# Performance work log

Measured on AMD Instinct MI355X. Metric: run time of the kernel, lower is better.

Reference implementation:

```python
import jax, jax.numpy as jnp
import numpy as np

D = 256            # number of graph nodes (example.size(3))
K1 = D // 2        # topkpool1 k
K2 = D // 4        # topkpool2 k
B = 8


def _lrelu(x):
    return jnp.where(x > 0, x, 0.33 * x)


def _e2e(h, wa, ba, wb, bb):
    # h: [B,C,d,d]; wa,wb: [P,C,d] (squeezed (1,d)/(d,1) conv kernels)
    # cnn1: contract over columns j -> [B,P,d]; cnn2: contract over rows i -> [B,P,d]
    a = jnp.einsum('bcij,pcj->bpi', h, wa) + ba[None, :, None]
    b = jnp.einsum('bcij,pci->bpj', h, wb) + bb[None, :, None]
    # cat([a]*d, 3) + cat([b]*d, 2)  ==  broadcast-add
    return a[:, :, :, None] + b[:, :, None, :]


def _gcn(h, g, W, b):
    # h: [B,N,F_in], g: [B,N,N]; faithful to norm_g: g[i,j] / deg[j] (column-normalized
    # because torch broadcasts the [N] degree vector over the LAST dim)
    gb = (g > 0).astype(h.dtype)
    deg = gb.sum(axis=2)                      # [B,N] row sums
    gn = gb / deg[:, None, :]                 # divide column j by deg[j]
    return jnp.einsum('bij,bjf->bif', gn, h) @ W.T + b


def _pool(h, g, s, k):
    # h: [B,N,F], g: [B,N,N], s: [B,N,1] -> top-k nodes by score (descending)
    vals, idx = jax.lax.top_k(s[:, :, 0], k)              # [B,k]
    hn = jnp.take_along_axis(h, idx[:, :, None], axis=1)  # [B,k,F]
    gn = jnp.take_along_axis(g, idx[:, :, None], axis=1)
    gn = jnp.take_along_axis(gn, idx[:, None, :], axis=2) # [B,k,k]
    return hn, gn, vals[:, :, None]


def _readout(h):
    # h: [B,N,F] (node axis = 1); torch ReadOut on [B,F,N,1] max/mean over dim=2
    return jnp.concatenate([h.max(axis=1), h.mean(axis=1)], axis=1)  # [B,2F]


def _forward(x, w1a, b1a, w1b, b1b, w2a, b2a, w2b, b2b, e2n_w, e2n_b,
             a11_w, a11_b, a12_w, a12_b, g1_w, g1_b,
             a21_w, a21_b, a22_w, a22_b,
             d1_w, d1_b, d2_w, d2_b, d3_w, d3_b):
    h = _lrelu(_e2e(x, w1a, b1a, w1b, b1b))         # [B,128,d,d]
    h = _lrelu(_e2e(h, w2a, b2a, w2b, b2b))         # [B,256,d,d]
    # E2N conv (1,d): [B,8,d,1] -> node features [B,d,8]
    nodes = _lrelu(jnp.einsum('bcij,pcj->bpi', h, e2n_w) + e2n_b[None, :, None])
    nodes = jnp.transpose(nodes, (0, 2, 1))          # [B,d,8]
    g0 = x[:, 0]                                     # [B,d,d]

    w = _lrelu(_gcn(nodes, g0, a11_w, a11_b))        # [B,d,1]
    w = jax.nn.sigmoid(_gcn(w, g0, a12_w, a12_b))
    h1, g1, s1 = _pool(nodes, g0, w, K1)             # [B,K1,8], [B,K1,K1], [B,K1,1]
    out = h1 * s1 + h1
    sum1 = _readout(out)                             # [B,16]

    h2 = _gcn(out, g1, g1_w, g1_b)                   # [B,K1,8] (no activation, as in torch)
    w = _lrelu(_gcn(h2, g1, a21_w, a21_b))
    w = jax.nn.sigmoid(_gcn(w, g1, a22_w, a22_b))
    h3, g2, s2 = _pool(h2, g1, w, K2)                # [B,K2,8]
    out2 = h3 * s2 + h3
    sum2 = _readout(out2)                            # [B,16]

    z = sum1 + sum2                                  # [B,16]
    z = _lrelu(z @ d1_w.T + d1_b)                    # dropout = identity (eval mode)
    z = _lrelu(z @ d2_w.T + d2_b)
    return z @ d3_w.T + d3_b                         # [B,1]


def setup_inputs() -> dict:
    key = jax.random.key(0)
    ks = jax.random.split(key, 16)
    f32 = jnp.float32

    def rn(k, shape, scale):
        return jax.random.normal(k, shape, dtype=f32) * scale

    return {
        'x': jax.random.normal(ks[0], (B, 1, D, D), dtype=f32),
        'w1a': rn(ks[1], (128, 1, D), 0.08),  'b1a': jnp.zeros((128,), f32),
        'w1b': rn(ks[2], (128, 1, D), 0.08),  'b1b': jnp.zeros((128,), f32),
        'w2a': rn(ks[3], (256, 128, D), 0.008), 'b2a': jnp.zeros((256,), f32),
        'w2b': rn(ks[4], (256, 128, D), 0.008), 'b2b': jnp.zeros((256,), f32),
        'e2n_w': rn(ks[5], (8, 256, D), 0.005), 'e2n_b': jnp.zeros((8,), f32),
        'a11_w': rn(ks[6], (1, 8), 0.3),  'a11_b': jnp.zeros((1,), f32),
        'a12_w': rn(ks[7], (1, 1), 0.3),  'a12_b': jnp.zeros((1,), f32),
        'g1_w': rn(ks[8], (8, 8), 0.3),   'g1_b': jnp.zeros((8,), f32),
        'a21_w': rn(ks[9], (1, 8), 0.3),  'a21_b': jnp.zeros((1,), f32),
        'a22_w': rn(ks[10], (1, 1), 0.3), 'a22_b': jnp.zeros((1,), f32),
        'd1_w': rn(ks[11], (128, 16), 0.2), 'd1_b': jnp.zeros((128,), f32),
        'd2_w': rn(ks[12], (64, 128), 0.08), 'd2_b': jnp.zeros((64,), f32),
        'd3_w': rn(ks[13], (1, 64), 0.1),  'd3_b': jnp.zeros((1,), f32),
    }


def reference(x, w1a, b1a, w1b, b1b, w2a, b2a, w2b, b2b, e2n_w, e2n_b,
              a11_w, a11_b, a12_w, a12_b, g1_w, g1_b,
              a21_w, a21_b, a22_w, a22_b,
              d1_w, d1_b, d2_w, d2_b, d3_w, d3_b):
    return _forward(x, w1a, b1a, w1b, b1b, w2a, b2a, w2b, b2b, e2n_w, e2n_b,
                    a11_w, a11_b, a12_w, a12_b, g1_w, g1_b,
                    a21_w, a21_b, a22_w, a22_b,
                    d1_w, d1_b, d2_w, d2_b, d3_w, d3_b)
```

## Files before the change

### kernel.cpp

```cpp
#include <hip/hip_runtime.h>
#include <hip/hip_bf16.h>

typedef short s16x8 __attribute__((ext_vector_type(8)));
typedef float f32x4 __attribute__((ext_vector_type(4)));
typedef float f32x2 __attribute__((ext_vector_type(2)));

#define TID threadIdx.x
#define N_IN 27

__device__ __forceinline__ float bf2f(unsigned short u) {
    unsigned v = ((unsigned)u) << 16;
    return __builtin_bit_cast(float, v);
}
__device__ __forceinline__ unsigned short f2bf(float f) {
    unsigned u = __builtin_bit_cast(unsigned, f);
    u += 0x7fffu + ((u >> 16) & 1u);
    return (unsigned short)(u >> 16);
}
__device__ __forceinline__ float lrelu_f(float x) { return fmaxf(x, 0.33f * x); }

__device__ __forceinline__ unsigned lrelu_pack(float pv, f32x2 q) {
    f32x2 s = q + pv;
    f32x2 m = s * 0.33f;
    f32x2 r = __builtin_elementwise_max(s, m);
    unsigned u;
    asm("v_cvt_pk_bf16_f32 %0, %1, %2" : "=v"(u) : "v"(r.x), "v"(r.y));
    return u;
}

union FragU { s16x8 v; uint4 q; unsigned w[4]; };

__global__ __launch_bounds__(256) void k_detect(const unsigned* __restrict__ w, int* __restrict__ flag) {
    __shared__ int cnt;
    if (TID == 0) cnt = 0;
    __syncthreads();
    int c = 0;
    for (int k = TID; k < 1024; k += 256) {
        unsigned e = (w[k] >> 23) & 0xFFu;
        c += (e >= 160u) ? 1 : 0;
    }
    atomicAdd(&cnt, c);
    __syncthreads();
    if (TID == 0) *flag = (cnt > 512) ? 1 : 0;
}

struct ConvArgs {
    const void* src[N_IN];
    unsigned short* dst[N_IN];
    int n[N_IN];
};

__global__ __launch_bounds__(256) void k_convert(ConvArgs A, const int* __restrict__ flag) {
    const int t = blockIdx.y;
    const int n = A.n[t];
    const int fl = *flag;
    if (fl && n >= 1000000) return;
    unsigned short* d = A.dst[t];
    const int npair = n >> 1;
    const int stride = gridDim.x * 256;
    if (fl) {
        const unsigned* s = (const unsigned*)A.src[t];
        for (int i = blockIdx.x * 256 + TID; i < npair; i += stride) ((unsigned*)d)[i] = s[i];
        if ((n & 1) && blockIdx.x == 0 && TID == 0) d[n - 1] = ((const unsigned short*)A.src[t])[n - 1];
    } else {
        const float* s = (const float*)A.src[t];
        for (int i = blockIdx.x * 256 + TID; i < npair; i += stride) {
            unsigned u;
            float a = s[2 * i], b = s[2 * i + 1];
            asm("v_cvt_pk_bf16_f32 %0, %1, %2" : "=v"(u) : "v"(a), "v"(b));
            ((unsigned*)d)[i] = u;
        }
        if ((n & 1) && blockIdx.x == 0 && TID == 0) d[n - 1] = f2bf(s[n - 1]);
    }
}

__global__ __launch_bounds__(128) void k_l1(
    const unsigned short* __restrict__ x,
    const unsigned short* __restrict__ w1a, const unsigned short* __restrict__ b1a,
    const unsigned short* __restrict__ w1b, const unsigned short* __restrict__ b1b,
    float* __restrict__ A1, float* __restrict__ B1)
{
    const int r = blockIdx.x, b = blockIdx.y, v = blockIdx.z;
    const int tid = TID;
    __shared__ float xr[256];
    const unsigned short* xb = x + b * 65536;
    if (v == 0) {
        xr[tid]       = bf2f(xb[r * 256 + tid]);
        xr[tid + 128] = bf2f(xb[r * 256 + tid + 128]);
    } else {
        xr[tid]       = bf2f(xb[tid * 256 + r]);
        xr[tid + 128] = bf2f(xb[(tid + 128) * 256 + r]);
    }
    __syncthreads();
    const unsigned short* w    = v ? w1b : w1a;
    const unsigned short* bias = v ? b1b : b1a;
    float* OUT = v ? B1 : A1;
    float acc = bf2f(bias[tid]);
    const unsigned short* wr = w + tid * 256;
    #pragma unroll 4
    for (int q = 0; q < 256; q += 8) {
        uint4 pk = *(const uint4*)(wr + q);
        unsigned ww0 = pk.x, ww1 = pk.y, ww2 = pk.z, ww3 = pk.w;
        acc += xr[q + 0] * bf2f((unsigned short)ww0) + xr[q + 1] * bf2f((unsigned short)(ww0 >> 16));
        acc += xr[q + 2] * bf2f((unsigned short)ww1) + xr[q + 3] * bf2f((unsigned short)(ww1 >> 16));
        acc += xr[q + 4] * bf2f((unsigned short)ww2) + xr[q + 5] * bf2f((unsigned short)(ww2 >> 16));
        acc += xr[q + 6] * bf2f((unsigned short)ww3) + xr[q + 7] * bf2f((unsigned short)(ww3 >> 16));
    }
    OUT[b * 32768 + tid * 256 + r] = acc;
}

__global__ __launch_bounds__(512) void k_e2e(
    const float* __restrict__ A1, const float* __restrict__ B1,
    const unsigned short* __restrict__ w2a_m, const unsigned short* __restrict__ w2b_m,
    const unsigned short* __restrict__ w2a_r, const unsigned short* __restrict__ w2b_r,
    const int* __restrict__ flag,
    float* __restrict__ part)
{
    const int rt = blockIdx.x;
    const int s  = blockIdx.y;
    const int bw = blockIdx.z;
    const int b = bw >> 1, which = bw & 1;
    const int fl = *flag;
    const float* P = (which ? B1 : A1) + b * 32768;
    const float* Q = (which ? A1 : B1) + b * 32768;
    const unsigned short* W = which ? (fl ? w2b_r : w2b_m) : (fl ? w2a_r : w2a_m);
    const int c0 = s * 16, r0 = rt * 128;

    __shared__ float Qs[16][256];
    __shared__ float Ps[16][128];

    const int tid = TID;
    {
        const float4* Qg = (const float4*)(Q + c0 * 256);
        float4* Qd = (float4*)&Qs[0][0];
        Qd[tid]       = Qg[tid];
        Qd[tid + 512] = Qg[tid + 512];
        int row = tid >> 5, col = tid & 31;
        *(float4*)&Ps[row][col * 4] = *(const float4*)&P[(c0 + row) * 256 + r0 + col * 4];
    }
    __syncthreads();

    const int wave = tid >> 6, lane = tid & 63, quad = lane >> 4, l16 = lane & 15;
    const int wi = wave & 3, wj = wave >> 2;
    const int pbase = wi * 64;
    const int rbase = wj * 64;

    f32x4 acc[4][4] = {};

    const unsigned short* Wrow[4];
    #pragma unroll
    for (int pf = 0; pf < 4; ++pf)
        Wrow[pf] = W + (size_t)(pbase + pf * 16 + l16) * 32768 + c0 * 256;

    for (int c = 0; c < 16; ++c) {
        float pv[4];
        #pragma unroll
        for (int nf = 0; nf < 4; ++nf) pv[nf] = Ps[c][rbase + nf * 16 + l16];
        #pragma unroll
        for (int q0 = 0; q0 < 8; ++q0) {
            const f32x2* qp = (const f32x2*)&Qs[c][q0 * 32 + quad * 8];
            FragU af[4];
            #pragma unroll
            for (int pf = 0; pf < 4; ++pf)
                af[pf].q = *(const uint4*)(Wrow[pf] + c * 256 + q0 * 32 + quad * 8);
            #pragma unroll
            for (int nf = 0; nf < 4; ++nf) {
                FragU hb;
                hb.w[0] = lrelu_pack(pv[nf], qp[0]);
                hb.w[1] = lrelu_pack(pv[nf], qp[1]);
                hb.w[2] = lrelu_pack(pv[nf], qp[2]);
                hb.w[3] = lrelu_pack(pv[nf], qp[3]);
                #pragma unroll
                for (int pf = 0; pf < 4; ++pf)
                    acc[pf][nf] = __builtin_amdgcn_mfma_f32_16x16x32_bf16(af[pf].v, hb.v, acc[pf][nf], 0, 0, 0);
            }
        }
    }
    float* pb = part + (size_t)(s * 16 + bw) * 65536;
    #pragma unroll
    for (int pf = 0; pf < 4; ++pf)
        #pragma unroll
        for (int nf = 0; nf < 4; ++nf)
            #pragma unroll
            for (int t = 0; t < 4; ++t) {
                int p = pbase + pf * 16 + quad * 4 + t;
                int r = r0 + rbase + nf * 16 + l16;
                pb[p * 256 + r] = acc[pf][nf][t];
            }
}

__global__ __launch_bounds__(256) void k_red(
    const float* __restrict__ part,
    const unsigned short* __restrict__ b2a, const unsigned short* __restrict__ b2b,
    float* __restrict__ A2, float* __restrict__ B2)
{
    const int bw = blockIdx.y; const int b = bw >> 1, which = bw & 1;
    const int idx = blockIdx.x * 256 + TID;
    const float4* pp = (const float4*)part;
    float4 acc = make_float4(0.f, 0.f, 0.f, 0.f);
    #pragma unroll
    for (int s = 0; s < 8; ++s) {
        float4 v = pp[(size_t)(s * 16 + bw) * 16384 + idx];
        acc.x += v.x; acc.y += v.y; acc.z += v.z; acc.w += v.w;
    }
    const int p = idx >> 6;
    const float bias = bf2f((which ? b2b : b2a)[p]);
    acc.x += bias; acc.y += bias; acc.z += bias; acc.w += bias;
    float* OUT = (which ? B2 : A2) + b * 65536;
    ((float4*)OUT)[idx] = acc;
}

__global__ __launch_bounds__(256) void k_e2n(
    const float* __restrict__ A2, const float* __restrict__ B2,
    const unsigned short* __restrict__ e2nw,
    float* __restrict__ nodes_raw)
{
    const int it = blockIdx.x, b = blockIdx.y, sn = blockIdx.z;
    const int tid = TID, wave = tid >> 6, lane = tid & 63, quad = lane >> 4, l16 = lane & 15;
    const int i0 = it * 16;
    const int c0 = sn * 32 + wave * 8;
    const float* Ab = A2 + b * 65536;
    const float* Bb = B2 + b * 65536;
    f32x4 acc = {};
    for (int cc = 0; cc < 8; ++cc) {
        const int c = c0 + cc;
        const float pv = Ab[c * 256 + i0 + l16];
        const float* Brow = Bb + c * 256;
        const unsigned short* Wrow = e2nw + (size_t)l16 * 65536 + c * 256;
        #pragma unroll
        for (int q0 = 0; q0 < 8; ++q0) {
            const f32x2* qp = (const f32x2*)&Brow[q0 * 32 + quad * 8];
            FragU a;
            if (l16 < 8) a.q = *(const uint4*)(Wrow + q0 * 32 + quad * 8);
            else         a.q = make_uint4(0u, 0u, 0u, 0u);
            FragU hb;
            hb.w[0] = lrelu_pack(pv, qp[0]);
            hb.w[1] = lrelu_pack(pv, qp[1]);
            hb.w[2] = lrelu_pack(pv, qp[2]);
            hb.w[3] = lrelu_pack(pv, qp[3]);
            acc = __builtin_amdgcn_mfma_f32_16x16x32_bf16(a.v, hb.v, acc, 0, 0, 0);
        }
    }
    __shared__ float red[4][16][16];
    #pragma unroll
    for (int t = 0; t < 4; ++t) red[wave][quad * 4 + t][l16] = acc[t];
    __syncthreads();
    const int row = tid >> 4, col = tid & 15;
    if (row < 8) {
        float ssum = red[0][row][col] + red[1][row][col] + red[2][row][col] + red[3][row][col];
        atomicAdd(&nodes_raw[b * 2048 + (i0 + col) * 8 + row], ssum);
    }
}

__global__ __launch_bounds__(256) void k_adj(
    const unsigned short* __restrict__ xm,
    unsigned long long* __restrict__ adjw, float* __restrict__ rdegw)
{
    const int b = blockIdx.y;
    const int tid = TID, wave = tid >> 6, lane = tid & 63;
    const int rbase = blockIdx.x * 32 + wave * 8;
    for (int rr = 0; rr < 8; ++rr) {
        const int row = rbase + rr;
        int d = 0;
        unsigned long long w[4];
        #pragma unroll
        for (int k = 0; k < 4; ++k) {
            float v = bf2f(xm[b * 65536 + row * 256 + k * 64 + lane]);
            w[k] = __ballot(v > 0.0f);
            d += __popcll(w[k]);
        }
        if (lane == 0) {
            #pragma unroll
            for (int k = 0; k < 4; ++k) adjw[(b * 256 + row) * 4 + k] = w[k];
            rdegw[b * 256 + row] = d ? 1.0f / (float)d : 0.0f;
        }
    }
}

__global__ __launch_bounds__(256) void k_tail(
    const unsigned long long* __restrict__ adjw, const float* __restrict__ rdegw,
    const float* __restrict__ nodes_raw, const unsigned short* __restrict__ e2n_b,
    const unsigned short* __restrict__ a11_w, const unsigned short* __restrict__ a11_b,
    const unsigned short* __restrict__ a12_w, const unsigned short* __restrict__ a12_b,
    const unsigned short* __restrict__ g1_w,  const unsigned short* __restrict__ g1_b,
    const unsigned short* __restrict__ a21_w, const unsigned short* __restrict__ a21_b,
    const unsigned short* __restrict__ a22_w, const unsigned short* __restrict__ a22_b,
    const unsigned short* __restrict__ d1_w,  const unsigned short* __restrict__ d1_b,
    const unsigned short* __restrict__ d2_w,  const unsigned short* __restrict__ d2_b,
    const unsigned short* __restrict__ d3_w,  const unsigned short* __restrict__ d3_b,
    const int* __restrict__ flag,
    void* __restrict__ outv)
{
    const int b = blockIdx.x;
    const int tid = TID;

    __shared__ unsigned long long adj[256][4];
    __shared__ float nod[256][8];
    __shared__ float rdeg[256];
    __shared__ float md[256];
    __shared__ float w1s[256];
    __shared__ float w2s[256];
    __shared__ int   selflag[256];
    __shared__ int   selidx[128];
    __shared__ float s1v[128];
    __shared__ float out1[128][8];
    __shared__ float aggL[128][8];
    __shared__ float h2L[128][8];
    __shared__ unsigned long long adj1[128][2];
    __shared__ float rdeg1[128];
    __shared__ float tA[128];
    __shared__ float w1t[128];
    __shared__ float w2t[128];
    __shared__ int   sel2flag[128];
    __shared__ int   sel2idx[64];
    __shared__ float s2v[64];
    __shared__ float out2[64][8];
    __shared__ float r1[16], r2[16], zz[16];
    __shared__ float z1[128];
    __shared__ float z2[64];

    if (tid < 128) { selidx[tid] = 0; s1v[tid] = 0.0f; }
    if (tid < 64)  { sel2idx[tid] = 0; s2v[tid] = 0.0f; }

    {
        #pragma unroll
        for (int k = 0; k < 4; ++k) adj[tid][k] = adjw[(b * 256 + tid) * 4 + k];
        rdeg[tid] = rdegw[b * 256 + tid];
        for (int f = 0; f < 8; ++f)
            nod[tid][f] = lrelu_f(nodes_raw[b * 2048 + tid * 8 + f] + bf2f(e2n_b[f]));
    }
    __syncthreads();
    {
        float s = 0.0f;
        for (int f = 0; f < 8; ++f) s += nod[tid][f] * bf2f(a11_w[f]);
        md[tid] = s * rdeg[tid];
    }
    __syncthreads();
    {
        float s = 0.0f;
        for (int k = 0; k < 4; ++k) {
            unsigned long long m = adj[tid][k];
            while (m) { int j = __builtin_ctzll(m); m &= m - 1; s += md[k * 64 + j]; }
        }
        w1s[tid] = lrelu_f(s + bf2f(a11_b[0]));
    }
    __syncthreads();
    md[tid] = w1s[tid] * bf2f(a12_w[0]) * rdeg[tid];
    __syncthreads();
    {
        float s = 0.0f;
        for (int k = 0; k < 4; ++k) {
            unsigned long long m = adj[tid][k];
            while (m) { int j = __builtin_ctzll(m); m &= m - 1; s += md[k * 64 + j]; }
        }
        w2s[tid] = 1.0f / (1.0f + expf(-(s + bf2f(a12_b[0]))));
    }
    __syncthreads();
    {
        const float my = w2s[tid];
        int cnt = 0;
        for (int j = 0; j < 256; ++j) {
            float o = w2s[j];
            cnt += (o > my) || (o == my && j < tid);
        }
        selflag[tid] = (cnt < 128) ? 1 : 0;
    }
    __syncthreads();
    if (selflag[tid]) {
        int pos = 0;
        for (int j = 0; j < tid; ++j) pos += selflag[j];
        if (pos < 128) { selidx[pos] = tid; s1v[pos] = w2s[tid]; }
    }
    __syncthreads();
    for (int k = tid; k < 1024; k += 256) {
        int t = k >> 3, f = k & 7;
        out1[t][f] = nod[selidx[t]][f] * (1.0f + s1v[t]);
    }
    __syncthreads();
    if (tid < 16) {
        int f = tid & 7;
        if (tid < 8) {
            float mx = -INFINITY;
            for (int t = 0; t < 128; ++t) mx = fmaxf(mx, out1[t][f]);
            r1[tid] = mx;
        } else {
            float s = 0.0f;
            for (int t = 0; t < 128; ++t) s += out1[t][f];
            r1[tid] = s * (1.0f / 128.0f);
        }
    }
    if (tid < 128) {
        unsigned long long wds[2] = {0ull, 0ull};
        const int gi = selidx[tid];
        for (int u = 0; u < 128; ++u) {
            const int gj = selidx[u];
            unsigned long long bit = (adj[gi][gj >> 6] >> (gj & 63)) & 1ull;
            wds[u >> 6] |= bit << (u & 63);
        }
        adj1[tid][0] = wds[0]; adj1[tid][1] = wds[1];
        int d = __popcll(wds[0]) + __popcll(wds[1]);
        rdeg1[tid] = d ? 1.0f / (float)d : 0.0f;
    }
    __syncthreads();
    {
        const int t = tid >> 1, f0 = (tid & 1) * 4;
        float a0 = 0, a1 = 0, a2 = 0, a3 = 0;
        for (int k = 0; k < 2; ++k) {
            unsigned long long m = adj1[t][k];
            while (m) {
                int u = __builtin_ctzll(m); m &= m - 1;
                int uu = k * 64 + u;
                float rr = rdeg1[uu];
                a0 += out1[uu][f0 + 0] * rr;
                a1 += out1[uu][f0 + 1] * rr;
                a2 += out1[uu][f0 + 2] * rr;
                a3 += out1[uu][f0 + 3] * rr;
            }
        }
        aggL[t][f0 + 0] = a0; aggL[t][f0 + 1] = a1; aggL[t][f0 + 2] = a2; aggL[t][f0 + 3] = a3;
    }
    __syncthreads();
    for (int k = tid; k < 1024; k += 256) {
        int t = k >> 3, fo = k & 7;
        float s = bf2f(g1_b[fo]);
        for (int f = 0; f < 8; ++f) s += aggL[t][f] * bf2f(g1_w[fo * 8 + f]);
        h2L[t][fo] = s;
    }
    __syncthreads();
    if (tid < 128) {
        float s = 0.0f;
        for (int f = 0; f < 8; ++f) s += h2L[tid][f] * bf2f(a21_w[f]);
        tA[tid] = s * rdeg1[tid];
    }
    __syncthreads();
    if (tid < 128) {
        float s = 0.0f;
        for (int k = 0; k < 2; ++k) {
            unsigned long long m = adj1[tid][k];
            while (m) { int u = __builtin_ctzll(m); m &= m - 1; s += tA[k * 64 + u]; }
        }
        w1t[tid] = lrelu_f(s + bf2f(a21_b[0]));
    }
    __syncthreads();
    if (tid < 128) tA[tid] = w1t[tid] * bf2f(a22_w[0]) * rdeg1[tid];
    __syncthreads();
    if (tid < 128) {
        float s = 0.0f;
        for (int k = 0; k < 2; ++k) {
            unsigned long long m = adj1[tid][k];
            while (m) { int u = __builtin_ctzll(m); m &= m - 1; s += tA[k * 64 + u]; }
        }
        w2t[tid] = 1.0f / (1.0f + expf(-(s + bf2f(a22_b[0]))));
    }
    __syncthreads();
    if (tid < 128) {
        const float my = w2t[tid];
        int cnt = 0;
        for (int u = 0; u < 128; ++u) {
            float o = w2t[u];
            cnt += (o > my) || (o == my && u < tid);
        }
        sel2flag[tid] = (cnt < 64) ? 1 : 0;
    }
    __syncthreads();
    if (tid < 128 && sel2flag[tid]) {
        int pos = 0;
        for (int u = 0; u < tid; ++u) pos += sel2flag[u];
        if (pos < 64) { sel2idx[pos] = tid; s2v[pos] = w2t[tid]; }
    }
    __syncthreads();
    for (int k = tid; k < 512; k += 256) {
        int u = k >> 3, f = k & 7;
        out2[u][f] = h2L[sel2idx[u]][f] * (1.0f + s2v[u]);
    }
    __syncthreads();
    if (tid < 16) {
        int f = tid & 7;
        if (tid < 8) {
            float mx = -INFINITY;
            for (int t = 0; t < 64; ++t) mx = fmaxf(mx, out2[t][f]);
            r2[tid] = mx;
        } else {
            float s = 0.0f;
            for (int t = 0; t < 64; ++t) s += out2[t][f];
            r2[tid] = s * (1.0f / 64.0f);
        }
    }
    __syncthreads();
    if (tid < 16) zz[tid] = r1[tid] + r2[tid];
    __syncthreads();
    if (tid < 128) {
        float s = bf2f(d1_b[tid]);
        for (int k = 0; k < 16; ++k) s += zz[k] * bf2f(d1_w[tid * 16 + k]);
        z1[tid] = lrelu_f(s);
    }
    __syncthreads();
    if (tid < 64) {
        float s = bf2f(d2_b[tid]);
        for (int k = 0; k < 128; ++k) s += z1[k] * bf2f(d2_w[tid * 128 + k]);
        z2[tid] = lrelu_f(s);
    }
    __syncthreads();
    if (tid == 0) {
        float s = bf2f(d3_b[0]);
        for (int k = 0; k < 64; ++k) s += z2[k] * bf2f(d3_w[k]);
        if (*flag) ((unsigned short*)outv)[b] = f2bf(s);
        else       ((float*)outv)[b] = s;
    }
}

extern "C" void kernel_launch(void* const* d_in, const int* in_sizes, int n_in,
                              void* d_out, int out_size, void* d_ws, size_t ws_size,
                              hipStream_t stream) {
    float* ws        = (float*)d_ws;
    float* A1        = ws;
    float* B1        = ws + 262144;
    float* A2        = ws + 524288;
    float* B2        = ws + 1048576;
    float* nodes_raw = ws + 1572864;
    float* rdegw     = ws + 1589248;
    int*   flag      = (int*)(ws + 1597440);
    unsigned long long* adjw = (unsigned long long*)(ws + 1597444);
    float* part      = ws + 1613832;
    unsigned short* mbase = (unsigned short*)(ws + 10002440);

    unsigned short* mir[N_IN];
    ConvArgs CA;
    {
        size_t off = 0;
        for (int i = 0; i < N_IN; ++i) {
            off = (off + 7) & ~(size_t)7;
            mir[i] = mbase + off;
            off += (size_t)in_sizes[i];
            CA.src[i] = d_in[i];
            CA.dst[i] = mir[i];
            CA.n[i]   = in_sizes[i];
        }
    }

    k_detect<<<dim3(1), 256, 0, stream>>>((const unsigned*)d_in[5], flag);
    k_convert<<<dim3(256, N_IN), 256, 0, stream>>>(CA, flag);
    hipMemsetAsync(nodes_raw, 0, 16384 * sizeof(float), stream);
    k_l1<<<dim3(256, 8, 2), 128, 0, stream>>>(mir[0], mir[1], mir[2], mir[3], mir[4], A1, B1);
    k_adj<<<dim3(8, 8), 256, 0, stream>>>(mir[0], adjw, rdegw);
    k_e2e<<<dim3(2, 8, 16), 512, 0, stream>>>(A1, B1,
        mir[5], mir[7],
        (const unsigned short*)d_in[5], (const unsigned short*)d_in[7],
        flag, part);
    k_red<<<dim3(64, 16), 256, 0, stream>>>(part, mir[6], mir[8], A2, B2);
    k_e2n<<<dim3(16, 8, 8), 256, 0, stream>>>(A2, B2, mir[9], nodes_raw);
    k_tail<<<dim3(8), 256, 0, stream>>>(adjw, rdegw, nodes_raw, mir[10],
        mir[11], mir[12], mir[13], mir[14], mir[15], mir[16], mir[17], mir[18],
        mir[19], mir[20], mir[21], mir[22], mir[23], mir[24], mir[25], mir[26],
        flag, d_out);
}
```

Before: 446.6 us.

## Drop dtype detection and full bf16 mirroring; convert only big weights; prefetch MFMA operands

Removes the input dtype detection kernel and the conversion of all 27 inputs to bf16. Only the large w2a, w2b and e2n weights are now converted, using vectorized float4 loads, and the small tensors and x are read as fp32 directly. The e2e and e2n MFMA loops now double-buffer the weight and Q fragments one step ahead, so load latency overlaps the matrix math. The trade-off is dropping support for bf16 inputs, plus extra register pressure from the prefetch buffers.

```diff
diff --git a/kernel.cpp b/kernel.cpp
--- a/kernel.cpp
+++ b/kernel.cpp
@@ -1,22 +1,11 @@
 #include <hip/hip_runtime.h>
-#include <hip/hip_bf16.h>
 
 typedef short s16x8 __attribute__((ext_vector_type(8)));
 typedef float f32x4 __attribute__((ext_vector_type(4)));
 typedef float f32x2 __attribute__((ext_vector_type(2)));
 
 #define TID threadIdx.x
-#define N_IN 27
-
-__device__ __forceinline__ float bf2f(unsigned short u) {
-    unsigned v = ((unsigned)u) << 16;
-    return __builtin_bit_cast(float, v);
-}
-__device__ __forceinline__ unsigned short f2bf(float f) {
-    unsigned u = __builtin_bit_cast(unsigned, f);
-    u += 0x7fffu + ((u >> 16) & 1u);
-    return (unsigned short)(u >> 16);
-}
+
 __device__ __forceinline__ float lrelu_f(float x) { return fmaxf(x, 0.33f * x); }
 
 __device__ __forceinline__ unsigned lrelu_pack(float pv, f32x2 q) {
@@ -27,103 +16,75 @@
     asm("v_cvt_pk_bf16_f32 %0, %1, %2" : "=v"(u) : "v"(r.x), "v"(r.y));
     return u;
 }
+__device__ __forceinline__ unsigned pk_bf16(float a, float b) {
+    unsigned u;
+    asm("v_cvt_pk_bf16_f32 %0, %1, %2" : "=v"(u) : "v"(a), "v"(b));
+    return u;
+}
 
 union FragU { s16x8 v; uint4 q; unsigned w[4]; };
 
-__global__ __launch_bounds__(256) void k_detect(const unsigned* __restrict__ w, int* __restrict__ flag) {
-    __shared__ int cnt;
-    if (TID == 0) cnt = 0;
-    __syncthreads();
-    int c = 0;
-    for (int k = TID; k < 1024; k += 256) {
-        unsigned e = (w[k] >> 23) & 0xFFu;
-        c += (e >= 160u) ? 1 : 0;
-    }
-    atomicAdd(&cnt, c);
-    __syncthreads();
-    if (TID == 0) *flag = (cnt > 512) ? 1 : 0;
-}
-
-struct ConvArgs {
-    const void* src[N_IN];
-    unsigned short* dst[N_IN];
-    int n[N_IN];
-};
-
-__global__ __launch_bounds__(256) void k_convert(ConvArgs A, const int* __restrict__ flag) {
-    const int t = blockIdx.y;
-    const int n = A.n[t];
-    const int fl = *flag;
-    if (fl && n >= 1000000) return;
-    unsigned short* d = A.dst[t];
-    const int npair = n >> 1;
+__global__ __launch_bounds__(256) void k_convert(
+    const float* __restrict__ sa, unsigned short* __restrict__ da, int na4,
+    const float* __restrict__ sb, unsigned short* __restrict__ db, int nb4,
+    const float* __restrict__ sc, unsigned short* __restrict__ dc, int nc4)
+{
+    const float* s; unsigned short* d; int n4;
+    if (blockIdx.y == 0)      { s = sa; d = da; n4 = na4; }
+    else if (blockIdx.y == 1) { s = sb; d = db; n4 = nb4; }
+    else                      { s = sc; d = dc; n4 = nc4; }
     const int stride = gridDim.x * 256;
-    if (fl) {
-        const unsigned* s = (const unsigned*)A.src[t];
-        for (int i = blockIdx.x * 256 + TID; i < npair; i += stride) ((unsigned*)d)[i] = s[i];
-        if ((n & 1) && blockIdx.x == 0 && TID == 0) d[n - 1] = ((const unsigned short*)A.src[t])[n - 1];
-    } else {
-        const float* s = (const float*)A.src[t];
-        for (int i = blockIdx.x * 256 + TID; i < npair; i += stride) {
-            unsigned u;
-            float a = s[2 * i], b = s[2 * i + 1];
-            asm("v_cvt_pk_bf16_f32 %0, %1, %2" : "=v"(u) : "v"(a), "v"(b));
-            ((unsigned*)d)[i] = u;
-        }
-        if ((n & 1) && blockIdx.x == 0 && TID == 0) d[n - 1] = f2bf(s[n - 1]);
+    for (int i = blockIdx.x * 256 + TID; i < n4; i += stride) {
+        float4 v = ((const float4*)s)[i];
+        ((uint2*)d)[i] = make_uint2(pk_bf16(v.x, v.y), pk_bf16(v.z, v.w));
     }
 }
 
 __global__ __launch_bounds__(128) void k_l1(
-    const unsigned short* __restrict__ x,
-    const unsigned short* __restrict__ w1a, const unsigned short* __restrict__ b1a,
-    const unsigned short* __restrict__ w1b, const unsigned short* __restrict__ b1b,
+    const float* __restrict__ x,
+    const float* __restrict__ w1a, const float* __restrict__ b1a,
+    const float* __restrict__ w1b, const float* __restrict__ b1b,
     float* __restrict__ A1, float* __restrict__ B1)
 {
     const int r = blockIdx.x, b = blockIdx.y, v = blockIdx.z;
     const int tid = TID;
     __shared__ float xr[256];
-    const unsigned short* xb = x + b * 65536;
+    const float* xb = x + b * 65536;
     if (v == 0) {
-        xr[tid]       = bf2f(xb[r * 256 + tid]);
-        xr[tid + 128] = bf2f(xb[r * 256 + tid + 128]);
+        xr[tid]       = xb[r * 256 + tid];
+        xr[tid + 128] = xb[r * 256 + tid + 128];
     } else {
-        xr[tid]       = bf2f(xb[tid * 256 + r]);
-        xr[tid + 128] = bf2f(xb[(tid + 128) * 256 + r]);
-    }
-    __syncthreads();
-    const unsigned short* w    = v ? w1b : w1a;
-    const unsigned short* bias = v ? b1b : b1a;
+        xr[tid]       = xb[tid * 256 + r];
+        xr[tid + 128] = xb[(tid + 128) * 256 + r];
+    }
+    __syncthreads();
+    const float* w    = v ? w1b : w1a;
+    const float* bias = v ? b1b : b1a;
     float* OUT = v ? B1 : A1;
-    float acc = bf2f(bias[tid]);
-    const unsigned short* wr = w + tid * 256;
+    float acc = bias[tid];
+    const float* wr = w + tid * 256;
     #pragma unroll 4
     for (int q = 0; q < 256; q += 8) {
-        uint4 pk = *(const uint4*)(wr + q);
-        unsigned ww0 = pk.x, ww1 = pk.y, ww2 = pk.z, ww3 = pk.w;
-        acc += xr[q + 0] * bf2f((unsigned short)ww0) + xr[q + 1] * bf2f((unsigned short)(ww0 >> 16));
-        acc += xr[q + 2] * bf2f((unsigned short)ww1) + xr[q + 3] * bf2f((unsigned short)(ww1 >> 16));
-        acc += xr[q + 4] * bf2f((unsigned short)ww2) + xr[q + 5] * bf2f((unsigned short)(ww2 >> 16));
-        acc += xr[q + 6] * bf2f((unsigned short)ww3) + xr[q + 7] * bf2f((unsigned short)(ww3 >> 16));
+        float4 a = *(const float4*)(wr + q);
+        float4 c = *(const float4*)(wr + q + 4);
+        acc += xr[q + 0] * a.x + xr[q + 1] * a.y + xr[q + 2] * a.z + xr[q + 3] * a.w;
+        acc += xr[q + 4] * c.x + xr[q + 5] * c.y + xr[q + 6] * c.z + xr[q + 7] * c.w;
     }
     OUT[b * 32768 + tid * 256 + r] = acc;
 }
 
 __global__ __launch_bounds__(512) void k_e2e(
     const float* __restrict__ A1, const float* __restrict__ B1,
-    const unsigned short* __restrict__ w2a_m, const unsigned short* __restrict__ w2b_m,
-    const unsigned short* __restrict__ w2a_r, const unsigned short* __restrict__ w2b_r,
-    const int* __restrict__ flag,
+    const unsigned short* __restrict__ w2aM, const unsigned short* __restrict__ w2bM,
     float* __restrict__ part)
 {
     const int rt = blockIdx.x;
     const int s  = blockIdx.y;
     const int bw = blockIdx.z;
     const int b = bw >> 1, which = bw & 1;
-    const int fl = *flag;
     const float* P = (which ? B1 : A1) + b * 32768;
     const float* Q = (which ? A1 : B1) + b * 32768;
-    const unsigned short* W = which ? (fl ? w2b_r : w2b_m) : (fl ? w2a_r : w2a_m);
+    const unsigned short* W = which ? w2bM : w2aM;
     const int c0 = s * 16, r0 = rt * 128;
 
     __shared__ float Qs[16][256];
@@ -142,37 +103,58 @@
 
     const int wave = tid >> 6, lane = tid & 63, quad = lane >> 4, l16 = lane & 15;
     const int wi = wave & 3, wj = wave >> 2;
-    const int pbase = wi * 64;
-    const int rbase = wj * 64;
+    const int pbase = wi * 64, rbase = wj * 64;
 
     f32x4 acc[4][4] = {};
 
     const unsigned short* Wrow[4];
     #pragma unroll
     for (int pf = 0; pf < 4; ++pf)
-        Wrow[pf] = W + (size_t)(pbase + pf * 16 + l16) * 32768 + c0 * 256;
+        Wrow[pf] = W + (size_t)(pbase + pf * 16 + l16) * 32768 + c0 * 256 + quad * 8;
+
+    FragU af[2][4];
+    f32x2 qp[2][4];
+    float pv[4], pvn[4];
+
+    #pragma unroll
+    for (int pf = 0; pf < 4; ++pf) af[0][pf].q = *(const uint4*)(Wrow[pf]);
+    #pragma unroll
+    for (int k = 0; k < 4; ++k) qp[0][k] = *(const f32x2*)&Qs[0][quad * 8 + 2 * k];
+    #pragma unroll
+    for (int nf = 0; nf < 4; ++nf) pv[nf] = Ps[0][rbase + nf * 16 + l16];
 
     for (int c = 0; c < 16; ++c) {
-        float pv[4];
-        #pragma unroll
-        for (int nf = 0; nf < 4; ++nf) pv[nf] = Ps[c][rbase + nf * 16 + l16];
         #pragma unroll
         for (int q0 = 0; q0 < 8; ++q0) {
-            const f32x2* qp = (const f32x2*)&Qs[c][q0 * 32 + quad * 8];
-            FragU af[4];
-            #pragma unroll
-            for (int pf = 0; pf < 4; ++pf)
-                af[pf].q = *(const uint4*)(Wrow[pf] + c * 256 + q0 * 32 + quad * 8);
+            const int cur = q0 & 1, nxt = cur ^ 1;
+            const int cn = (q0 == 7) ? c + 1 : c;
+            const int qn = (q0 + 1) & 7;
+            if (cn < 16) {
+                #pragma unroll
+                for (int pf = 0; pf < 4; ++pf)
+                    af[nxt][pf].q = *(const uint4*)(Wrow[pf] + cn * 256 + qn * 32);
+                #pragma unroll
+                for (int k = 0; k < 4; ++k)
+                    qp[nxt][k] = *(const f32x2*)&Qs[cn][qn * 32 + quad * 8 + 2 * k];
+            }
+            if (q0 == 4 && c + 1 < 16) {
+                #pragma unroll
+                for (int nf = 0; nf < 4; ++nf) pvn[nf] = Ps[c + 1][rbase + nf * 16 + l16];
+            }
             #pragma unroll
             for (int nf = 0; nf < 4; ++nf) {
                 FragU hb;
-                hb.w[0] = lrelu_pack(pv[nf], qp[0]);
-                hb.w[1] = lrelu_pack(pv[nf], qp[1]);
-                hb.w[2] = lrelu_pack(pv[nf], qp[2]);
-                hb.w[3] = lrelu_pack(pv[nf], qp[3]);
+                hb.w[0] = lrelu_pack(pv[nf], qp[cur][0]);
+                hb.w[1] = lrelu_pack(pv[nf], qp[cur][1]);
+                hb.w[2] = lrelu_pack(pv[nf], qp[cur][2]);
+                hb.w[3] = lrelu_pack(pv[nf], qp[cur][3]);
                 #pragma unroll
                 for (int pf = 0; pf < 4; ++pf)
-                    acc[pf][nf] = __builtin_amdgcn_mfma_f32_16x16x32_bf16(af[pf].v, hb.v, acc[pf][nf], 0, 0, 0);
+                    acc[pf][nf] = __builtin_amdgcn_mfma_f32_16x16x32_bf16(af[cur][pf].v, hb.v, acc[pf][nf], 0, 0, 0);
+            }
+            if (q0 == 7) {
+                #pragma unroll
+                for (int nf = 0; nf < 4; ++nf) pv[nf] = pvn[nf];
             }
         }
     }
@@ -191,7 +173,7 @@
 
 __global__ __launch_bounds__(256) void k_red(
     const float* __restrict__ part,
-    const unsigned short* __restrict__ b2a, const unsigned short* __restrict__ b2b,
+    const float* __restrict__ b2a, const float* __restrict__ b2b,
     float* __restrict__ A2, float* __restrict__ B2)
 {
     const int bw = blockIdx.y; const int b = bw >> 1, which = bw & 1;
@@ -204,7 +186,7 @@
         acc.x += v.x; acc.y += v.y; acc.z += v.z; acc.w += v.w;
     }
     const int p = idx >> 6;
-    const float bias = bf2f((which ? b2b : b2a)[p]);
+    const float bias = (which ? b2b : b2a)[p];
     acc.x += bias; acc.y += bias; acc.z += bias; acc.w += bias;
     float* OUT = (which ? B2 : A2) + b * 65536;
     ((float4*)OUT)[idx] = acc;
@@ -221,24 +203,41 @@
     const int c0 = sn * 32 + wave * 8;
     const float* Ab = A2 + b * 65536;
     const float* Bb = B2 + b * 65536;
+    const float* Brow0 = Bb + c0 * 256 + quad * 8;
+    const unsigned short* Wrow0 = e2nw + (size_t)l16 * 65536 + c0 * 256 + quad * 8;
+
     f32x4 acc = {};
+    FragU af[2];
+    f32x2 qp[2][4];
+    float pv, pvn;
+
+    if (l16 < 8) af[0].q = *(const uint4*)(Wrow0);
+    else         af[0].q = make_uint4(0u, 0u, 0u, 0u);
+    #pragma unroll
+    for (int k = 0; k < 4; ++k) qp[0][k] = *(const f32x2*)(Brow0 + 2 * k);
+    pv = Ab[c0 * 256 + i0 + l16];
+
     for (int cc = 0; cc < 8; ++cc) {
-        const int c = c0 + cc;
-        const float pv = Ab[c * 256 + i0 + l16];
-        const float* Brow = Bb + c * 256;
-        const unsigned short* Wrow = e2nw + (size_t)l16 * 65536 + c * 256;
         #pragma unroll
         for (int q0 = 0; q0 < 8; ++q0) {
-            const f32x2* qp = (const f32x2*)&Brow[q0 * 32 + quad * 8];
-            FragU a;
-            if (l16 < 8) a.q = *(const uint4*)(Wrow + q0 * 32 + quad * 8);
-            else         a.q = make_uint4(0u, 0u, 0u, 0u);
+            const int cur = q0 & 1, nxt = cur ^ 1;
+            const int cn = (q0 == 7) ? cc + 1 : cc;
+            const int qn = (q0 + 1) & 7;
+            if (cn < 8) {
+                if (l16 < 8) af[nxt].q = *(const uint4*)(Wrow0 + cn * 256 + qn * 32);
+                else         af[nxt].q = make_uint4(0u, 0u, 0u, 0u);
+                #pragma unroll
+                for (int k = 0; k < 4; ++k)
+                    qp[nxt][k] = *(const f32x2*)(Brow0 + cn * 256 + qn * 32 + 2 * k);
+            }
+            if (q0 == 4 && cc + 1 < 8) pvn = Ab[(c0 + cc + 1) * 256 + i0 + l16];
             FragU hb;
-            hb.w[0] = lrelu_pack(pv, qp[0]);
-            hb.w[1] = lrelu_pack(pv, qp[1]);
-            hb.w[2] = lrelu_pack(pv, qp[2]);
-            hb.w[3] = lrelu_pack(pv, qp[3]);
-            acc = __builtin_amdgcn_mfma_f32_16x16x32_bf16(a.v, hb.v, acc, 0, 0, 0);
+            hb.w[0] = lrelu_pack(pv, qp[cur][0]);
+            hb.w[1] = lrelu_pack(pv, qp[cur][1]);
+            hb.w[2] = lrelu_pack(pv, qp[cur][2]);
+            hb.w[3] = lrelu_pack(pv, qp[cur][3]);
+            acc = __builtin_amdgcn_mfma_f32_16x16x32_bf16(af[cur].v, hb.v, acc, 0, 0, 0);
+            if (q0 == 7) pv = pvn;
         }
     }
     __shared__ float red[4][16][16];
@@ -253,7 +252,7 @@
 }
 
 __global__ __launch_bounds__(256) void k_adj(
-    const unsigned short* __restrict__ xm,
+    const float* __restrict__ x,
     unsigned long long* __restrict__ adjw, float* __restrict__ rdegw)
 {
     const int b = blockIdx.y;
@@ -265,7 +264,7 @@
         unsigned long long w[4];
         #pragma unroll
         for (int k = 0; k < 4; ++k) {
-            float v = bf2f(xm[b * 65536 + row * 256 + k * 64 + lane]);
+            float v = x[b * 65536 + row * 256 + k * 64 + lane];
             w[k] = __ballot(v > 0.0f);
             d += __popcll(w[k]);
         }
@@ -279,17 +278,16 @@
 
 __global__ __launch_bounds__(256) void k_tail(
     const unsigned long long* __restrict__ adjw, const float* __restrict__ rdegw,
-    const float* __restrict__ nodes_raw, const unsigned short* __restrict__ e2n_b,
-    const unsigned short* __restrict__ a11_w, const unsigned short* __restrict__ a11_b,
-    const unsigned short* __restrict__ a12_w, const unsigned short* __restrict__ a12_b,
-    const unsigned short* __restrict__ g1_w,  const unsigned short* __restrict__ g1_b,
-    const unsigned short* __restrict__ a21_w, const unsigned short* __restrict__ a21_b,
-    const unsigned short* __restrict__ a22_w, const unsigned short* __restrict__ a22_b,
-    const unsigned short* __restrict__ d1_w,  const unsigned short* __restrict__ d1_b,
-    const unsigned short* __restrict__ d2_w,  const unsigned short* __restrict__ d2_b,
-    const unsigned short* __restrict__ d3_w,  const unsigned short* __restrict__ d3_b,
-    const int* __restrict__ flag,
-    void* __restrict__ outv)
+    const float* __restrict__ nodes_raw, const float* __restrict__ e2n_b,
+    const float* __restrict__ a11_w, const float* __restrict__ a11_b,
+    const float* __restrict__ a12_w, const float* __restrict__ a12_b,
+    const float* __restrict__ g1_w,  const float* __restrict__ g1_b,
+    const float* __restrict__ a21_w, const float* __restrict__ a21_b,
+    const float* __restrict__ a22_w, const float* __restrict__ a22_b,
+    const float* __restrict__ d1_w,  const float* __restrict__ d1_b,
+    const float* __restrict__ d2_w,  const float* __restrict__ d2_b,
+    const float* __restrict__ d3_w,  const float* __restrict__ d3_b,
+    float* __restrict__ out)
 {
     const int b = blockIdx.x;
     const int tid = TID;
@@ -327,12 +325,12 @@
         for (int k = 0; k < 4; ++k) adj[tid][k] = adjw[(b * 256 + tid) * 4 + k];
         rdeg[tid] = rdegw[b * 256 + tid];
         for (int f = 0; f < 8; ++f)
-            nod[tid][f] = lrelu_f(nodes_raw[b * 2048 + tid * 8 + f] + bf2f(e2n_b[f]));
+            nod[tid][f] = lrelu_f(nodes_raw[b * 2048 + tid * 8 + f] + e2n_b[f]);
     }
     __syncthreads();
     {
         float s = 0.0f;
-        for (int f = 0; f < 8; ++f) s += nod[tid][f] * bf2f(a11_w[f]);
+        for (int f = 0; f < 8; ++f) s += nod[tid][f] * a11_w[f];
         md[tid] = s * rdeg[tid];
     }
     __syncthreads();
@@ -342,10 +340,10 @@
             unsigned long long m = adj[tid][k];
             while (m) { int j = __builtin_ctzll(m); m &= m - 1; s += md[k * 64 + j]; }
         }
-        w1s[tid] = lrelu_f(s + bf2f(a11_b[0]));
-    }
-    __syncthreads();
-    md[tid] = w1s[tid] * bf2f(a12_w[0]) * rdeg[tid];
+        w1s[tid] = lrelu_f(s + a11_b[0]);
+    }
+    __syncthreads();
+    md[tid] = w1s[tid] * a12_w[0] * rdeg[tid];
     __syncthreads();
     {
         float s = 0.0f;
@@ -353,7 +351,7 @@
             unsigned long long m = adj[tid][k];
             while (m) { int j = __builtin_ctzll(m); m &= m - 1; s += md[k * 64 + j]; }
         }
-        w2s[tid] = 1.0f / (1.0f + expf(-(s + bf2f(a12_b[0]))));
+        w2s[tid] = 1.0f / (1.0f + expf(-(s + a12_b[0])));
     }
     __syncthreads();
     {
@@ -422,14 +420,14 @@
     __syncthreads();
     for (int k = tid; k < 1024; k += 256) {
         int t = k >> 3, fo = k & 7;
-        float s = bf2f(g1_b[fo]);
-        for (int f = 0; f < 8; ++f) s += aggL[t][f] * bf2f(g1_w[fo * 8 + f]);
+        float s = g1_b[fo];
+        for (int f = 0; f < 8; ++f) s += aggL[t][f] * g1_w[fo * 8 + f];
         h2L[t][fo] = s;
     }
     __syncthreads();
     if (tid < 128) {
         float s = 0.0f;
-        for (int f = 0; f < 8; ++f) s += h2L[tid][f] * bf2f(a21_w[f]);
+        for (int f = 0; f < 8; ++f) s += h2L[tid][f] * a21_w[f];
         tA[tid] = s * rdeg1[tid];
     }
     __syncthreads();
@@ -439,10 +437,10 @@
             unsigned long long m = adj1[tid][k];
             while (m) { int u = __builtin_ctzll(m); m &= m - 1; s += tA[k * 64 + u]; }
         }
-        w1t[tid] = lrelu_f(s + bf2f(a21_b[0]));
-    }
-    __syncthreads();
-    if (tid < 128) tA[tid] = w1t[tid] * bf2f(a22_w[0]) * rdeg1[tid];
+        w1t[tid] = lrelu_f(s + a21_b[0]);
+    }
+    __syncthreads();
+    if (tid < 128) tA[tid] = w1t[tid] * a22_w[0] * rdeg1[tid];
     __syncthreads();
     if (tid < 128) {
         float s = 0.0f;
@@ -450,7 +448,7 @@
             unsigned long long m = adj1[tid][k];
             while (m) { int u = __builtin_ctzll(m); m &= m - 1; s += tA[k * 64 + u]; }
         }
-        w2t[tid] = 1.0f / (1.0f + expf(-(s + bf2f(a22_b[0]))));
+        w2t[tid] = 1.0f / (1.0f + expf(-(s + a22_b[0])));
     }
     __syncthreads();
     if (tid < 128) {
@@ -490,28 +488,38 @@
     if (tid < 16) zz[tid] = r1[tid] + r2[tid];
     __syncthreads();
     if (tid < 128) {
-        float s = bf2f(d1_b[tid]);
-        for (int k = 0; k < 16; ++k) s += zz[k] * bf2f(d1_w[tid * 16 + k]);
+        float s = d1_b[tid];
+        for (int k = 0; k < 16; ++k) s += zz[k] * d1_w[tid * 16 + k];
         z1[tid] = lrelu_f(s);
     }
     __syncthreads();
     if (tid < 64) {
-        float s = bf2f(d2_b[tid]);
-        for (int k = 0; k < 128; ++k) s += z1[k] * bf2f(d2_w[tid * 128 + k]);
+        float s = d2_b[tid];
+        for (int k = 0; k < 128; ++k) s += z1[k] * d2_w[tid * 128 + k];
         z2[tid] = lrelu_f(s);
     }
     __syncthreads();
     if (tid == 0) {
-        float s = bf2f(d3_b[0]);
-        for (int k = 0; k < 64; ++k) s += z2[k] * bf2f(d3_w[k]);
-        if (*flag) ((unsigned short*)outv)[b] = f2bf(s);
-        else       ((float*)outv)[b] = s;
+        float s = d3_b[0];
+        for (int k = 0; k < 64; ++k) s += z2[k] * d3_w[k];
+        out[b] = s;
     }
 }
 
 extern "C" void kernel_launch(void* const* d_in, const int* in_sizes, int n_in,
                               void* d_out, int out_size, void* d_ws, size_t ws_size,
                               hipStream_t stream) {
+    const float* x     = (const float*)d_in[0];
+    const float* w1a   = (const float*)d_in[1];
+    const float* b1a   = (const float*)d_in[2];
+    const float* w1b   = (const float*)d_in[3];
+    const float* b1b   = (const float*)d_in[4];
+    const float* w2a   = (const float*)d_in[5];
+    const float* b2a   = (const float*)d_in[6];
+    const float* w2b   = (const float*)d_in[7];
+    const float* b2b   = (const float*)d_in[8];
+    const float* e2nw  = (const float*)d_in[9];
+
     float* ws        = (float*)d_ws;
     float* A1        = ws;
     float* B1        = ws + 262144;
@@ -519,38 +527,26 @@
     float* B2        = ws + 1048576;
     float* nodes_raw = ws + 1572864;
     float* rdegw     = ws + 1589248;
-    int*   flag      = (int*)(ws + 1597440);
-    unsigned long long* adjw = (unsigned long long*)(ws + 1597444);
-    float* part      = ws + 1613832;
-    unsigned short* mbase = (unsigned short*)(ws + 10002440);
-
-    unsigned short* mir[N_IN];
-    ConvArgs CA;
-    {
-        size_t off = 0;
-        for (int i = 0; i < N_IN; ++i) {
-            off = (off + 7) & ~(size_t)7;
-            mir[i] = mbase + off;
-            off += (size_t)in_sizes[i];
-            CA.src[i] = d_in[i];
-            CA.dst[i] = mir[i];
-            CA.n[i]   = in_sizes[i];
-        }
-    }
-
-    k_detect<<<dim3(1), 256, 0, stream>>>((const unsigned*)d_in[5], flag);
-    k_convert<<<dim3(256, N_IN), 256, 0, stream>>>(CA, flag);
+    unsigned long long* adjw = (unsigned long long*)(ws + 1597440);
+    float* part      = ws + 1613824;
+    unsigned short* w2aM  = (unsigned short*)(ws + 10002432);
+    unsigned short* w2bM  = w2aM + 8388608;
+    unsigned short* e2nwM = w2bM + 8388608;
+
+    k_convert<<<dim3(512, 3), 256, 0, stream>>>(
+        w2a, w2aM, 8388608 / 4,
+        w2b, w2bM, 8388608 / 4,
+        e2nw, e2nwM, 524288 / 4);
     hipMemsetAsync(nodes_raw, 0, 16384 * sizeof(float), stream);
-    k_l1<<<dim3(256, 8, 2), 128, 0, stream>>>(mir[0], mir[1], mir[2], mir[3], mir[4], A1, B1);
-    k_adj<<<dim3(8, 8), 256, 0, stream>>>(mir[0], adjw, rdegw);
-    k_e2e<<<dim3(2, 8, 16), 512, 0, stream>>>(A1, B1,
-        mir[5], mir[7],
-        (const unsigned short*)d_in[5], (const unsigned short*)d_in[7],
-        flag, part);
-    k_red<<<dim3(64, 16), 256, 0, stream>>>(part, mir[6], mir[8], A2, B2);
-    k_e2n<<<dim3(16, 8, 8), 256, 0, stream>>>(A2, B2, mir[9], nodes_raw);
-    k_tail<<<dim3(8), 256, 0, stream>>>(adjw, rdegw, nodes_raw, mir[10],
-        mir[11], mir[12], mir[13], mir[14], mir[15], mir[16], mir[17], mir[18],
-        mir[19], mir[20], mir[21], mir[22], mir[23], mir[24], mir[25], mir[26],
-        flag, d_out);
-}
+    k_l1<<<dim3(256, 8, 2), 128, 0, stream>>>(x, w1a, b1a, w1b, b1b, A1, B1);
+    k_adj<<<dim3(8, 8), 256, 0, stream>>>(x, adjw, rdegw);
+    k_e2e<<<dim3(2, 8, 16), 512, 0, stream>>>(A1, B1, w2aM, w2bM, part);
+    k_red<<<dim3(64, 16), 256, 0, stream>>>(part, b2a, b2b, A2, B2);
+    k_e2n<<<dim3(16, 8, 8), 256, 0, stream>>>(A2, B2, e2nwM, nodes_raw);
+    k_tail<<<dim3(8), 256, 0, stream>>>(adjw, rdegw, nodes_raw, (const float*)d_in[10],
+        (const float*)d_in[11], (const float*)d_in[12], (const float*)d_in[13], (const float*)d_in[14],
+        (const float*)d_in[15], (const float*)d_in[16], (const float*)d_in[17], (const float*)d_in[18],
+        (const float*)d_in[19], (const float*)d_in[20], (const float*)d_in[21], (const float*)d_in[22],
+        (const float*)d_in[23], (const float*)d_in[24], (const float*)d_in[25], (const float*)d_in[26],
+        (float*)d_out);
+}
```

Measured after the change: 438.6 us. Within noise of the previous version (-1.8%).
